# Kernel tuning notes

Hardware: AMD Instinct MI355X
Metric: run time of the kernel (lower is better)

The kernel has to match this reference:

```python
import jax, jax.numpy as jnp
import numpy as np

B, S, D_IN = 32, 4096, 256
D, T, NB, K = 256, 256, 4, 5  # d_model, compressed_len, n_blocks, kernel_size
EPS = 1e-5


def setup_inputs() -> dict:
    key = jax.random.key(0)
    ks = jax.random.split(key, 20)
    x = jax.random.normal(ks[0], (B, S, D_IN), jnp.float32)
    # ragged valid-prefix lengths in [1, S]
    lengths = jax.random.randint(ks[1], (B,), 1, S + 1)
    mask = jnp.arange(S)[None, :] < lengths[:, None]  # bool [B,S]
    sc = 0.02
    inp = {
        'x': x,
        'mask': mask,
        'in_w': jax.random.normal(ks[2], (D_IN, D), jnp.float32) * sc,
        'in_b': jnp.zeros((D,), jnp.float32),
        'ln_g': jnp.ones((NB, D), jnp.float32),
        'ln_b': jnp.zeros((NB, D), jnp.float32),
        'dw_w': jax.random.normal(ks[3], (NB, D, 1, K), jnp.float32) * sc,
        'dw_b': jnp.zeros((NB, D), jnp.float32),
        'win_w': jax.random.normal(ks[4], (NB, D, 2 * D), jnp.float32) * sc,
        'win_b': jnp.zeros((NB, 2 * D), jnp.float32),
        'wout_w': jax.random.normal(ks[5], (NB, D, D), jnp.float32) * sc,
        'wout_b': jnp.zeros((NB, D), jnp.float32),
        'fn_g': jnp.ones((D,), jnp.float32),
        'fn_b': jnp.zeros((D,), jnp.float32),
    }
    return inp


def layer_norm(h, g, b):
    mu = jnp.mean(h, axis=-1, keepdims=True)
    var = jnp.mean((h - mu) ** 2, axis=-1, keepdims=True)
    return (h - mu) * jax.lax.rsqrt(var + EPS) * g + b


def compress(x, mask, target_len):
    # Vectorized equivalent of the per-sample F.interpolate(mode='linear',
    # align_corners=False) loop: src = (j+0.5)*(L/T) - 0.5, clamped, lerp.
    lengths = mask.astype(jnp.int32).sum(axis=1)  # [B]
    Lf = lengths.astype(x.dtype)
    j = jnp.arange(target_len, dtype=x.dtype)
    src = (j[None, :] + 0.5) * (Lf[:, None] / target_len) - 0.5  # [B,T]
    src = jnp.clip(src, 0.0, jnp.maximum(Lf[:, None] - 1.0, 0.0))
    i0 = jnp.floor(src).astype(jnp.int32)
    i1 = jnp.minimum(i0 + 1, jnp.maximum(lengths[:, None] - 1, 0))
    w = (src - i0.astype(x.dtype))[..., None]  # [B,T,1]
    gather = jax.vmap(lambda xb, ib: xb[ib])  # [S,D],[T] -> [T,D]
    out = (1.0 - w) * gather(x, i0) + w * gather(x, i1)  # [B,T,D]
    valid = lengths > 0
    out = jnp.where(valid[:, None, None], out, 0.0)
    comp_mask = jnp.broadcast_to(valid[:, None], (x.shape[0], target_len))
    return out, comp_mask


def conv_block(h, g, b, dww, dwb, winw, winb, woutw, woutb):
    residual = h
    hn = layer_norm(h, g, b)
    hc = jax.lax.conv_general_dilated(
        hn.transpose(0, 2, 1), dww, window_strides=(1,),
        padding=[(K // 2, K // 2)], dimension_numbers=('NCW', 'OIW', 'NCW'),
        feature_group_count=D)
    hc = hc.transpose(0, 2, 1) + dwb  # [B,T,D]
    gv = hc @ winw + winb
    gate, val = jnp.split(gv, 2, axis=-1)
    h2 = jax.nn.sigmoid(gate) * jax.nn.gelu(val, approximate=False)
    return residual + h2 @ woutw + woutb


def reference(x, mask, in_w, in_b, ln_g, ln_b, dw_w, dw_b, win_w, win_b,
              wout_w, wout_b, fn_g, fn_b):
    xc, comp_mask = compress(x, mask, T)
    h = xc @ in_w + in_b
    for i in range(NB):
        h = conv_block(h, ln_g[i], ln_b[i], dw_w[i], dw_b[i], win_w[i],
                       win_b[i], wout_w[i], wout_b[i])
    return layer_norm(h, fn_g, fn_b), comp_mask
```

## Files before the change

kernel.cpp:

```cpp
#include <hip/hip_runtime.h>
#include <math.h>

#define B_    32
#define S_    4096
#define DIN_  256
#define D_    256
#define T_    256
#define NB_   4
#define K_    5
#define EPS_  1e-5f
#define ROWS_ (B_ * T_)

#define MROWS 32
#define GROWS 36
#define ASTR  264

typedef short  shortx8 __attribute__((ext_vector_type(8)));
typedef float  floatx4 __attribute__((ext_vector_type(4)));

__device__ __forceinline__ unsigned short f2bf(float f) {
    unsigned int u = __float_as_uint(f);
    u += 0x7FFFu + ((u >> 16) & 1u);
    return (unsigned short)(u >> 16);
}
__device__ __forceinline__ float bf2f(unsigned short h) {
    return __uint_as_float(((unsigned int)h) << 16);
}

__global__ void k_setup(const float* __restrict__ in_w, const float* __restrict__ win_w,
                        const float* __restrict__ wout_w, const unsigned int* __restrict__ mask_w,
                        unsigned short* __restrict__ wt_in, unsigned short* __restrict__ wt_win,
                        unsigned short* __restrict__ wt_wout, int* __restrict__ lengths) {
    int z = blockIdx.z;
    int tid = threadIdx.x;

    if (z == 9) {
        int b = blockIdx.y * 16 + blockIdx.x;
        if (b >= B_) return;
        int mode = 0;
        unsigned int w0 = mask_w[0];
        if (w0 == 0x3F800000u) mode = 2;
        else {
            bool u8 = false;
            for (int i = 0; i < 32; ++i)
                if (mask_w[i * 1024] > 1u) { u8 = true; break; }
            mode = u8 ? 1 : 0;
        }
        int s = 0;
        if (mode == 0) {
            const int* m = (const int*)mask_w;
            for (int i = tid; i < S_; i += 256) s += (m[(size_t)b * S_ + i] != 0);
        } else if (mode == 2) {
            const float* m = (const float*)mask_w;
            for (int i = tid; i < S_; i += 256) s += (m[(size_t)b * S_ + i] != 0.0f);
        } else {
            const unsigned char* m = (const unsigned char*)mask_w;
            for (int i = tid; i < S_; i += 256) s += (m[(size_t)b * S_ + i] != 0);
        }
        __shared__ int sm[256];
        sm[tid] = s;
        __syncthreads();
        for (int off = 128; off > 0; off >>= 1) {
            if (tid < off) sm[tid] += sm[tid + off];
            __syncthreads();
        }
        if (tid == 0) lengths[b] = sm[0];
        return;
    }

    const float* src; unsigned short* dst; int N, Kd;
    if (z == 0)      { src = in_w;                                   dst = wt_in;                                   N = D_;     Kd = DIN_; }
    else if (z <= 4) { src = win_w  + (size_t)(z - 1) * D_ * 2 * D_; dst = wt_win  + (size_t)(z - 1) * 2 * D_ * D_; N = 2 * D_; Kd = D_; }
    else             { src = wout_w + (size_t)(z - 5) * D_ * D_;     dst = wt_wout + (size_t)(z - 5) * D_ * D_;     N = D_;     Kd = D_; }
    int bx = blockIdx.x * 32;
    int by = blockIdx.y * 32;
    if (bx >= N) return;
    __shared__ float tile[32][33];
    int tx = tid & 31, ty = tid >> 5;
#pragma unroll
    for (int i = 0; i < 32; i += 8)
        tile[ty + i][tx] = src[(size_t)(by + ty + i) * N + bx + tx];
    __syncthreads();
#pragma unroll
    for (int i = 0; i < 32; i += 8)
        dst[(size_t)(bx + ty + i) * Kd + by + tx] = f2bf(tile[tx][ty + i]);
}

template<bool INIT>
__device__ __forceinline__ void gemm2(
    const unsigned short (*A)[ASTR], const unsigned short* __restrict__ wt,
    const float* __restrict__ bias, float (&hreg)[2][2][4],
    int w, int c16, int q)
{
#pragma unroll
    for (int nn = 0; nn < 2; ++nn) {
        int nt = w + nn * 8;
        const unsigned short* wp = wt + (size_t)(nt * 16 + c16) * 256 + q * 8;
        shortx8 Bf[8];
#pragma unroll
        for (int kk = 0; kk < 8; ++kk) Bf[kk] = *(const shortx8*)(wp + kk * 32);
        floatx4 acc[2] = {};
#pragma unroll
        for (int kk = 0; kk < 8; ++kk) {
#pragma unroll
            for (int mt = 0; mt < 2; ++mt) {
                shortx8 a = *(const shortx8*)&A[2 + mt * 16 + c16][kk * 32 + q * 8];
                acc[mt] = __builtin_amdgcn_mfma_f32_16x16x32_bf16(a, Bf[kk], acc[mt], 0, 0, 0);
            }
        }
        float ob = bias[nt * 16 + c16];
#pragma unroll
        for (int mt = 0; mt < 2; ++mt)
#pragma unroll
            for (int r = 0; r < 4; ++r) {
                float v = acc[mt][r] + ob;
                if (INIT) hreg[nn][mt][r] = v; else hreg[nn][mt][r] += v;
            }
    }
}

__device__ __forceinline__ void stats_pass(
    const float (&hreg)[2][2][4], float2* st,
    float (*rowS)[MROWS], float (*rowSS)[MROWS],
    int tid, int w, int c16, int q)
{
#pragma unroll
    for (int mt = 0; mt < 2; ++mt)
#pragma unroll
        for (int r = 0; r < 4; ++r) {
            float v0 = hreg[0][mt][r], v1 = hreg[1][mt][r];
            float s = v0 + v1, ss = v0 * v0 + v1 * v1;
#pragma unroll
            for (int off = 1; off < 16; off <<= 1) {
                s += __shfl_xor(s, off);
                ss += __shfl_xor(ss, off);
            }
            if (c16 == 0) {
                rowS[w][mt * 16 + q * 4 + r] = s;
                rowSS[w][mt * 16 + q * 4 + r] = ss;
            }
        }
    __syncthreads();
    if (tid < MROWS) {
        float s = 0.f, ss = 0.f;
#pragma unroll
        for (int i = 0; i < 8; ++i) { s += rowS[i][tid]; ss += rowSS[i][tid]; }
        float mu = s * (1.0f / D_);
        float var = ss * (1.0f / D_) - mu * mu;
        st[tid] = make_float2(mu, rsqrtf(var + EPS_));
    }
    __syncthreads();
}

__global__ __launch_bounds__(512, 4) void k_mega(
    const float* __restrict__ x, const int* __restrict__ lengths,
    const unsigned short* __restrict__ wt_in, const float* __restrict__ in_b,
    const float* __restrict__ ln_g, const float* __restrict__ ln_b,
    const float* __restrict__ dw_w, const float* __restrict__ dw_b,
    const unsigned short* __restrict__ wt_win, const float* __restrict__ win_b,
    const unsigned short* __restrict__ wt_wout, const float* __restrict__ wout_b,
    const float* __restrict__ fn_g, const float* __restrict__ fn_b,
    float* __restrict__ out0, float* __restrict__ out1)
{
    __shared__ unsigned short buf0[GROWS][ASTR];
    __shared__ unsigned short buf1[GROWS][ASTR];
    __shared__ float2 st[MROWS];
    __shared__ float rowS[8][MROWS];
    __shared__ float rowSS[8][MROWS];

    int tid = threadIdx.x;
    int w = tid >> 6, lane = tid & 63;
    int c16 = lane & 15, q = lane >> 4;
    int bid = blockIdx.x;
    int b = bid >> 4, seg = bid & 15;
    int t0 = seg * 16 - 8;
    if (t0 < 0) t0 = 0;
    if (t0 > T_ - MROWS) t0 = T_ - MROWS;
    int out_lo = seg * 16;

    float hreg[2][2][4];
    int L = lengths[b];

    {
        int ccol = tid & 255, r0 = tid >> 8;
        float Lf = (float)L;
        float hi = fmaxf(Lf - 1.0f, 0.0f);
        int L1 = max(L - 1, 0);
        const float* xb = x + (size_t)b * S_ * DIN_ + ccol;
#pragma unroll
        for (int e = 0; e < 16; ++e) {
            int row = r0 + e * 2;
            int t = t0 + row;
            float src = ((float)t + 0.5f) * (Lf * (1.0f / T_)) - 0.5f;
            src = fminf(fmaxf(src, 0.0f), hi);
            int i0 = (int)floorf(src);
            int i1 = min(i0 + 1, L1);
            float wf = src - (float)i0;
            float v0 = xb[(size_t)i0 * DIN_];
            float v1 = xb[(size_t)i1 * DIN_];
            buf0[2 + row][ccol] = f2bf((1.0f - wf) * v0 + wf * v1);
        }
    }
    __syncthreads();

    gemm2<true>(buf0, wt_in, in_b, hreg, w, c16, q);

    for (int li = 0; li < NB_; ++li) {
        const float* g_i = ln_g + li * D_;
        const float* b_i = ln_b + li * D_;
        const float* dww = dw_w + li * D_ * K_;
        const float* dwb = dw_b + li * D_;
        const unsigned short* ww = wt_win + (size_t)li * 2 * D_ * D_;
        const float* wb = win_b + li * 2 * D_;
        const unsigned short* ow = wt_wout + (size_t)li * D_ * D_;
        const float* ob = wout_b + li * D_;

        stats_pass(hreg, st, rowS, rowSS, tid, w, c16, q);

#pragma unroll
        for (int nn = 0; nn < 2; ++nn) {
            int col = (w + nn * 8) * 16 + c16;
            float gg = g_i[col], bb = b_i[col];
#pragma unroll
            for (int mt = 0; mt < 2; ++mt)
#pragma unroll
                for (int r = 0; r < 4; ++r) {
                    int row = mt * 16 + q * 4 + r;
                    float2 s = st[row];
                    buf0[2 + row][col] = f2bf((hreg[nn][mt][r] - s.x) * s.y * gg + bb);
                }
        }
        {
            int idx = tid;
#pragma unroll
            for (int zz = 0; zz < 2; ++zz, idx += 512) {
                int gr = idx >> 8;
                int p = (gr < 2) ? gr : gr + 32;
                buf0[p][idx & 255] = 0;
            }
        }
        __syncthreads();

        {
            int ccol = tid & 255, r0 = tid >> 8;
            float wk[K_];
#pragma unroll
            for (int k = 0; k < K_; ++k) wk[k] = dww[ccol * K_ + k];
            float cb = dwb[ccol];
#pragma unroll
            for (int e = 0; e < 16; ++e) {
                int row = r0 + e * 2;
                float acc = cb;
#pragma unroll
                for (int k = 0; k < K_; ++k)
                    acc += bf2f(buf0[row + k][ccol]) * wk[k];
                buf1[2 + row][ccol] = f2bf(acc);
            }
        }
        __syncthreads();

        float gvreg[4][2][4];
#pragma unroll
        for (int nn = 0; nn < 4; ++nn) {
            int nt = w + nn * 8;
            const unsigned short* wp = ww + (size_t)(nt * 16 + c16) * 256 + q * 8;
            shortx8 Bf[8];
#pragma unroll
            for (int kk = 0; kk < 8; ++kk) Bf[kk] = *(const shortx8*)(wp + kk * 32);
            floatx4 acc[2] = {};
#pragma unroll
            for (int kk = 0; kk < 8; ++kk) {
#pragma unroll
                for (int mt = 0; mt < 2; ++mt) {
                    shortx8 a = *(const shortx8*)&buf1[2 + mt * 16 + c16][kk * 32 + q * 8];
                    acc[mt] = __builtin_amdgcn_mfma_f32_16x16x32_bf16(a, Bf[kk], acc[mt], 0, 0, 0);
                }
            }
            float bb = wb[nt * 16 + c16];
#pragma unroll
            for (int mt = 0; mt < 2; ++mt)
#pragma unroll
                for (int r = 0; r < 4; ++r) gvreg[nn][mt][r] = acc[mt][r] + bb;
        }

#pragma unroll
        for (int pp = 0; pp < 2; ++pp) {
            int col = (w + pp * 8) * 16 + c16;
#pragma unroll
            for (int mt = 0; mt < 2; ++mt)
#pragma unroll
                for (int r = 0; r < 4; ++r) {
                    float gate = gvreg[pp][mt][r];
                    float val  = gvreg[pp + 2][mt][r];
                    float sg = 1.0f / (1.0f + __expf(-gate));
                    float u = 1.5957691216f * (val + 0.044715f * val * val * val);
                    float ge = val / (1.0f + __expf(-u));
                    buf0[2 + mt * 16 + q * 4 + r][col] = f2bf(sg * ge);
                }
        }
        __syncthreads();

        gemm2<false>(buf0, ow, ob, hreg, w, c16, q);
    }

    stats_pass(hreg, st, rowS, rowSS, tid, w, c16, q);
#pragma unroll
    for (int nn = 0; nn < 2; ++nn) {
        int col = (w + nn * 8) * 16 + c16;
        float gg = fn_g[col], bb = fn_b[col];
#pragma unroll
        for (int mt = 0; mt < 2; ++mt)
#pragma unroll
            for (int r = 0; r < 4; ++r) {
                int row = mt * 16 + q * 4 + r;
                int t = t0 + row;
                int tl = t - out_lo;
                if (tl >= 0 && tl < 16) {
                    float2 s = st[row];
                    out0[((size_t)b * T_ + t) * D_ + col] =
                        (hreg[nn][mt][r] - s.x) * s.y * gg + bb;
                }
            }
    }
    if (tid < 16) out1[(size_t)b * T_ + out_lo + tid] = 1.0f;
}

extern "C" void kernel_launch(void* const* d_in, const int* in_sizes, int n_in,
                              void* d_out, int out_size, void* d_ws, size_t ws_size,
                              hipStream_t stream) {
    const float* x      = (const float*)d_in[0];
    const unsigned int* mask_w = (const unsigned int*)d_in[1];
    const float* in_w   = (const float*)d_in[2];
    const float* in_b   = (const float*)d_in[3];
    const float* ln_g   = (const float*)d_in[4];
    const float* ln_b   = (const float*)d_in[5];
    const float* dw_w   = (const float*)d_in[6];
    const float* dw_b   = (const float*)d_in[7];
    const float* win_w  = (const float*)d_in[8];
    const float* win_b  = (const float*)d_in[9];
    const float* wout_w = (const float*)d_in[10];
    const float* wout_b = (const float*)d_in[11];
    const float* fn_g   = (const float*)d_in[12];
    const float* fn_b   = (const float*)d_in[13];

    char* w8 = (char*)d_ws;
    unsigned short* wt_in   = (unsigned short*)w8;
    unsigned short* wt_win  = wt_in  + (size_t)D_ * DIN_;
    unsigned short* wt_wout = wt_win + (size_t)NB_ * 2 * D_ * D_;
    int* lengths = (int*)(w8 + (4u << 20));

    float* out0 = (float*)d_out;
    float* out1 = out0 + (size_t)ROWS_ * D_;

    k_setup<<<dim3(16, 8, 10), 256, 0, stream>>>(in_w, win_w, wout_w, mask_w,
                                                 wt_in, wt_win, wt_wout, lengths);
    k_mega<<<512, 512, 0, stream>>>(x, lengths, wt_in, in_b, ln_g, ln_b, dw_w, dw_b,
                                    wt_win, win_b, wt_wout, wout_b, fn_g, fn_b,
                                    out0, out1);
}
```

Baseline: 312.8 us.

## Split fused mega-kernel into per-block kernels with global h and halo exchange

Replaces the single fused kernel, which used overlapping 32-row tiles (16 useful rows plus halo) so each block could carry the whole 4-block stack, with a front kernel and one kernel per conv block. Activations round-trip through global fp32 buffers, and each block recomputes LayerNorm for its 2-row halo. This removes the redundant halo compute (half the rows were wasted) and halves the grid. It also prefetches the next weight fragments while the current MFMA tile runs and packs the depthwise conv into two columns per thread. The cost is extra global traffic per layer and five launches, at lower occupancy (launch bounds 2).

```diff
diff --git a/kernel.cpp b/kernel.cpp
--- a/kernel.cpp
+++ b/kernel.cpp
@@ -11,8 +11,8 @@
 #define EPS_  1e-5f
 #define ROWS_ (B_ * T_)
 
-#define MROWS 32
-#define GROWS 36
+#define ORS_  32
+#define HR_   36
 #define ASTR  264
 
 typedef short  shortx8 __attribute__((ext_vector_type(8)));
@@ -23,8 +23,11 @@
     u += 0x7FFFu + ((u >> 16) & 1u);
     return (unsigned short)(u >> 16);
 }
-__device__ __forceinline__ float bf2f(unsigned short h) {
-    return __uint_as_float(((unsigned int)h) << 16);
+__device__ __forceinline__ float bf2f_lo(unsigned int u) {
+    return __uint_as_float(u << 16);
+}
+__device__ __forceinline__ float bf2f_hi(unsigned int u) {
+    return __uint_as_float(u & 0xFFFF0000u);
 }
 
 __global__ void k_setup(const float* __restrict__ in_w, const float* __restrict__ win_w,
@@ -86,107 +89,24 @@
         dst[(size_t)(bx + ty + i) * Kd + by + tx] = f2bf(tile[tx][ty + i]);
 }
 
-template<bool INIT>
-__device__ __forceinline__ void gemm2(
-    const unsigned short (*A)[ASTR], const unsigned short* __restrict__ wt,
-    const float* __restrict__ bias, float (&hreg)[2][2][4],
-    int w, int c16, int q)
-{
-#pragma unroll
-    for (int nn = 0; nn < 2; ++nn) {
-        int nt = w + nn * 8;
-        const unsigned short* wp = wt + (size_t)(nt * 16 + c16) * 256 + q * 8;
-        shortx8 Bf[8];
-#pragma unroll
-        for (int kk = 0; kk < 8; ++kk) Bf[kk] = *(const shortx8*)(wp + kk * 32);
-        floatx4 acc[2] = {};
-#pragma unroll
-        for (int kk = 0; kk < 8; ++kk) {
-#pragma unroll
-            for (int mt = 0; mt < 2; ++mt) {
-                shortx8 a = *(const shortx8*)&A[2 + mt * 16 + c16][kk * 32 + q * 8];
-                acc[mt] = __builtin_amdgcn_mfma_f32_16x16x32_bf16(a, Bf[kk], acc[mt], 0, 0, 0);
-            }
-        }
-        float ob = bias[nt * 16 + c16];
-#pragma unroll
-        for (int mt = 0; mt < 2; ++mt)
-#pragma unroll
-            for (int r = 0; r < 4; ++r) {
-                float v = acc[mt][r] + ob;
-                if (INIT) hreg[nn][mt][r] = v; else hreg[nn][mt][r] += v;
-            }
-    }
-}
-
-__device__ __forceinline__ void stats_pass(
-    const float (&hreg)[2][2][4], float2* st,
-    float (*rowS)[MROWS], float (*rowSS)[MROWS],
-    int tid, int w, int c16, int q)
-{
-#pragma unroll
-    for (int mt = 0; mt < 2; ++mt)
-#pragma unroll
-        for (int r = 0; r < 4; ++r) {
-            float v0 = hreg[0][mt][r], v1 = hreg[1][mt][r];
-            float s = v0 + v1, ss = v0 * v0 + v1 * v1;
-#pragma unroll
-            for (int off = 1; off < 16; off <<= 1) {
-                s += __shfl_xor(s, off);
-                ss += __shfl_xor(ss, off);
-            }
-            if (c16 == 0) {
-                rowS[w][mt * 16 + q * 4 + r] = s;
-                rowSS[w][mt * 16 + q * 4 + r] = ss;
-            }
-        }
-    __syncthreads();
-    if (tid < MROWS) {
-        float s = 0.f, ss = 0.f;
-#pragma unroll
-        for (int i = 0; i < 8; ++i) { s += rowS[i][tid]; ss += rowSS[i][tid]; }
-        float mu = s * (1.0f / D_);
-        float var = ss * (1.0f / D_) - mu * mu;
-        st[tid] = make_float2(mu, rsqrtf(var + EPS_));
-    }
-    __syncthreads();
-}
-
-__global__ __launch_bounds__(512, 4) void k_mega(
+__global__ __launch_bounds__(512, 2) void k_front(
     const float* __restrict__ x, const int* __restrict__ lengths,
     const unsigned short* __restrict__ wt_in, const float* __restrict__ in_b,
-    const float* __restrict__ ln_g, const float* __restrict__ ln_b,
-    const float* __restrict__ dw_w, const float* __restrict__ dw_b,
-    const unsigned short* __restrict__ wt_win, const float* __restrict__ win_b,
-    const unsigned short* __restrict__ wt_wout, const float* __restrict__ wout_b,
-    const float* __restrict__ fn_g, const float* __restrict__ fn_b,
-    float* __restrict__ out0, float* __restrict__ out1)
+    float* __restrict__ h0)
 {
-    __shared__ unsigned short buf0[GROWS][ASTR];
-    __shared__ unsigned short buf1[GROWS][ASTR];
-    __shared__ float2 st[MROWS];
-    __shared__ float rowS[8][MROWS];
-    __shared__ float rowSS[8][MROWS];
-
+    __shared__ unsigned short bufC[ORS_][ASTR];
     int tid = threadIdx.x;
     int w = tid >> 6, lane = tid & 63;
     int c16 = lane & 15, q = lane >> 4;
-    int bid = blockIdx.x;
-    int b = bid >> 4, seg = bid & 15;
-    int t0 = seg * 16 - 8;
-    if (t0 < 0) t0 = 0;
-    if (t0 > T_ - MROWS) t0 = T_ - MROWS;
-    int out_lo = seg * 16;
-
-    float hreg[2][2][4];
+    int b = blockIdx.x >> 3, seg = blockIdx.x & 7;
+    int t0 = seg * ORS_;
     int L = lengths[b];
-
     {
-        int ccol = tid & 255, r0 = tid >> 8;
+        int col = tid & 255, r0 = tid >> 8;
         float Lf = (float)L;
         float hi = fmaxf(Lf - 1.0f, 0.0f);
         int L1 = max(L - 1, 0);
-        const float* xb = x + (size_t)b * S_ * DIN_ + ccol;
+        const float* xb = x + (size_t)b * S_ * DIN_ + col;
 #pragma unroll
         for (int e = 0; e < 16; ++e) {
             int row = r0 + e * 2;
@@ -198,131 +118,268 @@
             float wf = src - (float)i0;
             float v0 = xb[(size_t)i0 * DIN_];
             float v1 = xb[(size_t)i1 * DIN_];
-            buf0[2 + row][ccol] = f2bf((1.0f - wf) * v0 + wf * v1);
+            bufC[row][col] = f2bf((1.0f - wf) * v0 + wf * v1);
         }
     }
     __syncthreads();
-
-    gemm2<true>(buf0, wt_in, in_b, hreg, w, c16, q);
-
-    for (int li = 0; li < NB_; ++li) {
-        const float* g_i = ln_g + li * D_;
-        const float* b_i = ln_b + li * D_;
-        const float* dww = dw_w + li * D_ * K_;
-        const float* dwb = dw_b + li * D_;
-        const unsigned short* ww = wt_win + (size_t)li * 2 * D_ * D_;
-        const float* wb = win_b + li * 2 * D_;
-        const unsigned short* ow = wt_wout + (size_t)li * D_ * D_;
-        const float* ob = wout_b + li * D_;
-
-        stats_pass(hreg, st, rowS, rowSS, tid, w, c16, q);
-
+#pragma unroll
+    for (int nn = 0; nn < 2; ++nn) {
+        int nt = w + nn * 8;
+        const unsigned short* wp = wt_in + (size_t)(nt * 16 + c16) * 256 + q * 8;
+        shortx8 Bf[8];
+#pragma unroll
+        for (int kk = 0; kk < 8; ++kk) Bf[kk] = *(const shortx8*)(wp + kk * 32);
+        floatx4 acc[2] = {};
+#pragma unroll
+        for (int kk = 0; kk < 8; ++kk)
+#pragma unroll
+            for (int mt = 0; mt < 2; ++mt) {
+                shortx8 a = *(const shortx8*)&bufC[mt * 16 + c16][kk * 32 + q * 8];
+                acc[mt] = __builtin_amdgcn_mfma_f32_16x16x32_bf16(a, Bf[kk], acc[mt], 0, 0, 0);
+            }
+        float ob = in_b[nt * 16 + c16];
+#pragma unroll
+        for (int mt = 0; mt < 2; ++mt)
+#pragma unroll
+            for (int r = 0; r < 4; ++r) {
+                int row = mt * 16 + q * 4 + r;
+                h0[((size_t)b * T_ + t0 + row) * D_ + nt * 16 + c16] = acc[mt][r] + ob;
+            }
+    }
+}
+
+__global__ __launch_bounds__(512, 2) void k_blk(
+    const float* __restrict__ hin, float* __restrict__ hout,
+    const float* __restrict__ g_i, const float* __restrict__ b_i,
+    const float* __restrict__ dww, const float* __restrict__ dwb,
+    const unsigned short* __restrict__ ww, const float* __restrict__ wb,
+    const unsigned short* __restrict__ ow, const float* __restrict__ ob,
+    const float* __restrict__ fn_g, const float* __restrict__ fn_b,
+    float* __restrict__ out0, float* __restrict__ out1, int last)
+{
+    __shared__ unsigned short buf0[HR_][ASTR];
+    __shared__ unsigned short buf1[ORS_][ASTR];
+    __shared__ float2 st[ORS_];
+    __shared__ float rowS[8][ORS_];
+    __shared__ float rowSS[8][ORS_];
+
+    int tid = threadIdx.x;
+    int w = tid >> 6, lane = tid & 63;
+    int c16 = lane & 15, q = lane >> 4;
+    int b = blockIdx.x >> 3, seg = blockIdx.x & 7;
+    int t0 = seg * ORS_;
+
+    {
+        float gv4[4], bv4[4];
+#pragma unroll
+        for (int i = 0; i < 4; ++i) { gv4[i] = g_i[lane + 64 * i]; bv4[i] = b_i[lane + 64 * i]; }
+        float vv[5][4];
+#pragma unroll
+        for (int it = 0; it < 5; ++it) {
+            int r = w + it * 8;
+            int t = t0 - 2 + r;
+            bool ok = (r < HR_) && (t >= 0) && (t < T_);
+            int tc = min(max(t, 0), T_ - 1);
+            const float* hp = hin + ((size_t)b * T_ + tc) * D_ + lane;
+#pragma unroll
+            for (int i = 0; i < 4; ++i) {
+                float v = hp[64 * i];
+                vv[it][i] = ok ? v : 0.0f;
+            }
+        }
+#pragma unroll
+        for (int it = 0; it < 5; ++it) {
+            int r = w + it * 8;
+            if (r < HR_) {
+                float s  = vv[it][0] + vv[it][1] + vv[it][2] + vv[it][3];
+                float ss = vv[it][0] * vv[it][0] + vv[it][1] * vv[it][1]
+                         + vv[it][2] * vv[it][2] + vv[it][3] * vv[it][3];
+#pragma unroll
+                for (int off = 1; off < 64; off <<= 1) {
+                    s += __shfl_xor(s, off);
+                    ss += __shfl_xor(ss, off);
+                }
+                float mu = s * (1.0f / D_);
+                float rsig = rsqrtf(ss * (1.0f / D_) - mu * mu + EPS_);
+                int t = t0 - 2 + r;
+                bool okt = (t >= 0) && (t < T_);
+#pragma unroll
+                for (int i = 0; i < 4; ++i) {
+                    float ln = (vv[it][i] - mu) * rsig * gv4[i] + bv4[i];
+                    buf0[r][lane + 64 * i] = okt ? f2bf(ln) : (unsigned short)0;
+                }
+            }
+        }
+    }
+    shortx8 Bf[8];
+    {
+        const unsigned short* wp = ww + (size_t)(w * 16 + c16) * 256 + q * 8;
+#pragma unroll
+        for (int kk = 0; kk < 8; ++kk) Bf[kk] = *(const shortx8*)(wp + kk * 32);
+    }
+    __syncthreads();
+
+    {
+        int cp = tid & 127;
+        int rg = tid >> 7;
+        int col = cp * 2;
+        float wk0[K_], wk1[K_];
+#pragma unroll
+        for (int k = 0; k < K_; ++k) { wk0[k] = dww[col * K_ + k]; wk1[k] = dww[(col + 1) * K_ + k]; }
+        float cb0 = dwb[col], cb1 = dwb[col + 1];
+#pragma unroll
+        for (int e = 0; e < 8; ++e) {
+            int rr = rg + e * 4;
+            float a0 = cb0, a1 = cb1;
+#pragma unroll
+            for (int k = 0; k < K_; ++k) {
+                unsigned int u = *(const unsigned int*)&buf0[rr + k][col];
+                a0 += bf2f_lo(u) * wk0[k];
+                a1 += bf2f_hi(u) * wk1[k];
+            }
+            unsigned int o = ((unsigned int)f2bf(a0)) | (((unsigned int)f2bf(a1)) << 16);
+            *(unsigned int*)&buf1[rr][col] = o;
+        }
+    }
+    __syncthreads();
+
+    float gvreg[4][2][4];
+#pragma unroll
+    for (int nn = 0; nn < 4; ++nn) {
+        shortx8 Bn[8];
+        if (nn < 3) {
+            const unsigned short* wp = ww + (size_t)((w + (nn + 1) * 8) * 16 + c16) * 256 + q * 8;
+#pragma unroll
+            for (int kk = 0; kk < 8; ++kk) Bn[kk] = *(const shortx8*)(wp + kk * 32);
+        } else {
+            const unsigned short* wp = ow + (size_t)(w * 16 + c16) * 256 + q * 8;
+#pragma unroll
+            for (int kk = 0; kk < 8; ++kk) Bn[kk] = *(const shortx8*)(wp + kk * 32);
+        }
+        floatx4 acc[2] = {};
+#pragma unroll
+        for (int kk = 0; kk < 8; ++kk)
+#pragma unroll
+            for (int mt = 0; mt < 2; ++mt) {
+                shortx8 a = *(const shortx8*)&buf1[mt * 16 + c16][kk * 32 + q * 8];
+                acc[mt] = __builtin_amdgcn_mfma_f32_16x16x32_bf16(a, Bf[kk], acc[mt], 0, 0, 0);
+            }
+        float bb = wb[(w + nn * 8) * 16 + c16];
+#pragma unroll
+        for (int mt = 0; mt < 2; ++mt)
+#pragma unroll
+            for (int r = 0; r < 4; ++r) gvreg[nn][mt][r] = acc[mt][r] + bb;
+#pragma unroll
+        for (int kk = 0; kk < 8; ++kk) Bf[kk] = Bn[kk];
+    }
+#pragma unroll
+    for (int pp = 0; pp < 2; ++pp) {
+        int colw = (w + pp * 8) * 16 + c16;
+#pragma unroll
+        for (int mt = 0; mt < 2; ++mt)
+#pragma unroll
+            for (int r = 0; r < 4; ++r) {
+                float gate = gvreg[pp][mt][r];
+                float val  = gvreg[pp + 2][mt][r];
+                float sg = 1.0f / (1.0f + __expf(-gate));
+                float u = 1.5957691216f * (val + 0.044715f * val * val * val);
+                float ge = val / (1.0f + __expf(-u));
+                buf0[mt * 16 + q * 4 + r][colw] = f2bf(sg * ge);
+            }
+    }
+    __syncthreads();
+
+    float vreg[2][2][4];
+#pragma unroll
+    for (int nn = 0; nn < 2; ++nn) {
+        int nt = w + nn * 8;
+        shortx8 Bn[8];
+        if (nn == 0) {
+            const unsigned short* wp = ow + (size_t)((w + 8) * 16 + c16) * 256 + q * 8;
+#pragma unroll
+            for (int kk = 0; kk < 8; ++kk) Bn[kk] = *(const shortx8*)(wp + kk * 32);
+        }
+        float res[2][4];
+#pragma unroll
+        for (int mt = 0; mt < 2; ++mt)
+#pragma unroll
+            for (int r = 0; r < 4; ++r) {
+                int row = mt * 16 + q * 4 + r;
+                res[mt][r] = hin[((size_t)b * T_ + t0 + row) * D_ + nt * 16 + c16];
+            }
+        floatx4 acc[2] = {};
+#pragma unroll
+        for (int kk = 0; kk < 8; ++kk)
+#pragma unroll
+            for (int mt = 0; mt < 2; ++mt) {
+                shortx8 a = *(const shortx8*)&buf0[mt * 16 + c16][kk * 32 + q * 8];
+                acc[mt] = __builtin_amdgcn_mfma_f32_16x16x32_bf16(a, Bf[kk], acc[mt], 0, 0, 0);
+            }
+        float bb = ob[nt * 16 + c16];
+#pragma unroll
+        for (int mt = 0; mt < 2; ++mt)
+#pragma unroll
+            for (int r = 0; r < 4; ++r)
+                vreg[nn][mt][r] = res[mt][r] + acc[mt][r] + bb;
+        if (nn == 0) {
+#pragma unroll
+            for (int kk = 0; kk < 8; ++kk) Bf[kk] = Bn[kk];
+        }
+    }
+
+    if (!last) {
+#pragma unroll
+        for (int nn = 0; nn < 2; ++nn)
+#pragma unroll
+            for (int mt = 0; mt < 2; ++mt)
+#pragma unroll
+                for (int r = 0; r < 4; ++r) {
+                    int row = mt * 16 + q * 4 + r;
+                    hout[((size_t)b * T_ + t0 + row) * D_ + (w + nn * 8) * 16 + c16] = vreg[nn][mt][r];
+                }
+    } else {
+#pragma unroll
+        for (int mt = 0; mt < 2; ++mt)
+#pragma unroll
+            for (int r = 0; r < 4; ++r) {
+                float s = vreg[0][mt][r] + vreg[1][mt][r];
+                float ss = vreg[0][mt][r] * vreg[0][mt][r] + vreg[1][mt][r] * vreg[1][mt][r];
+#pragma unroll
+                for (int off = 1; off < 16; off <<= 1) {
+                    s += __shfl_xor(s, off);
+                    ss += __shfl_xor(ss, off);
+                }
+                if (c16 == 0) {
+                    rowS[w][mt * 16 + q * 4 + r] = s;
+                    rowSS[w][mt * 16 + q * 4 + r] = ss;
+                }
+            }
+        __syncthreads();
+        if (tid < ORS_) {
+            float s = 0.f, ss = 0.f;
+#pragma unroll
+            for (int i = 0; i < 8; ++i) { s += rowS[i][tid]; ss += rowSS[i][tid]; }
+            float mu = s * (1.0f / D_);
+            float var = ss * (1.0f / D_) - mu * mu;
+            st[tid] = make_float2(mu, rsqrtf(var + EPS_));
+        }
+        __syncthreads();
 #pragma unroll
         for (int nn = 0; nn < 2; ++nn) {
             int col = (w + nn * 8) * 16 + c16;
-            float gg = g_i[col], bb = b_i[col];
+            float gg = fn_g[col], bb = fn_b[col];
 #pragma unroll
             for (int mt = 0; mt < 2; ++mt)
 #pragma unroll
                 for (int r = 0; r < 4; ++r) {
                     int row = mt * 16 + q * 4 + r;
-                    float2 s = st[row];
-                    buf0[2 + row][col] = f2bf((hreg[nn][mt][r] - s.x) * s.y * gg + bb);
-                }
-        }
-        {
-            int idx = tid;
-#pragma unroll
-            for (int zz = 0; zz < 2; ++zz, idx += 512) {
-                int gr = idx >> 8;
-                int p = (gr < 2) ? gr : gr + 32;
-                buf0[p][idx & 255] = 0;
-            }
-        }
-        __syncthreads();
-
-        {
-            int ccol = tid & 255, r0 = tid >> 8;
-            float wk[K_];
-#pragma unroll
-            for (int k = 0; k < K_; ++k) wk[k] = dww[ccol * K_ + k];
-            float cb = dwb[ccol];
-#pragma unroll
-            for (int e = 0; e < 16; ++e) {
-                int row = r0 + e * 2;
-                float acc = cb;
-#pragma unroll
-                for (int k = 0; k < K_; ++k)
-                    acc += bf2f(buf0[row + k][ccol]) * wk[k];
-                buf1[2 + row][ccol] = f2bf(acc);
-            }
-        }
-        __syncthreads();
-
-        float gvreg[4][2][4];
-#pragma unroll
-        for (int nn = 0; nn < 4; ++nn) {
-            int nt = w + nn * 8;
-            const unsigned short* wp = ww + (size_t)(nt * 16 + c16) * 256 + q * 8;
-            shortx8 Bf[8];
-#pragma unroll
-            for (int kk = 0; kk < 8; ++kk) Bf[kk] = *(const shortx8*)(wp + kk * 32);
-            floatx4 acc[2] = {};
-#pragma unroll
-            for (int kk = 0; kk < 8; ++kk) {
-#pragma unroll
-                for (int mt = 0; mt < 2; ++mt) {
-                    shortx8 a = *(const shortx8*)&buf1[2 + mt * 16 + c16][kk * 32 + q * 8];
-                    acc[mt] = __builtin_amdgcn_mfma_f32_16x16x32_bf16(a, Bf[kk], acc[mt], 0, 0, 0);
-                }
-            }
-            float bb = wb[nt * 16 + c16];
-#pragma unroll
-            for (int mt = 0; mt < 2; ++mt)
-#pragma unroll
-                for (int r = 0; r < 4; ++r) gvreg[nn][mt][r] = acc[mt][r] + bb;
-        }
-
-#pragma unroll
-        for (int pp = 0; pp < 2; ++pp) {
-            int col = (w + pp * 8) * 16 + c16;
-#pragma unroll
-            for (int mt = 0; mt < 2; ++mt)
-#pragma unroll
-                for (int r = 0; r < 4; ++r) {
-                    float gate = gvreg[pp][mt][r];
-                    float val  = gvreg[pp + 2][mt][r];
-                    float sg = 1.0f / (1.0f + __expf(-gate));
-                    float u = 1.5957691216f * (val + 0.044715f * val * val * val);
-                    float ge = val / (1.0f + __expf(-u));
-                    buf0[2 + mt * 16 + q * 4 + r][col] = f2bf(sg * ge);
-                }
-        }
-        __syncthreads();
-
-        gemm2<false>(buf0, ow, ob, hreg, w, c16, q);
-    }
-
-    stats_pass(hreg, st, rowS, rowSS, tid, w, c16, q);
-#pragma unroll
-    for (int nn = 0; nn < 2; ++nn) {
-        int col = (w + nn * 8) * 16 + c16;
-        float gg = fn_g[col], bb = fn_b[col];
-#pragma unroll
-        for (int mt = 0; mt < 2; ++mt)
-#pragma unroll
-            for (int r = 0; r < 4; ++r) {
-                int row = mt * 16 + q * 4 + r;
-                int t = t0 + row;
-                int tl = t - out_lo;
-                if (tl >= 0 && tl < 16) {
-                    float2 s = st[row];
-                    out0[((size_t)b * T_ + t) * D_ + col] =
-                        (hreg[nn][mt][r] - s.x) * s.y * gg + bb;
-                }
-            }
-    }
-    if (tid < 16) out1[(size_t)b * T_ + out_lo + tid] = 1.0f;
+                    float2 sv = st[row];
+                    out0[((size_t)b * T_ + t0 + row) * D_ + col] =
+                        (vreg[nn][mt][r] - sv.x) * sv.y * gg + bb;
+                }
+        }
+        if (tid < ORS_) out1[(size_t)b * T_ + t0 + tid] = 1.0f;
+    }
 }
 
 extern "C" void kernel_launch(void* const* d_in, const int* in_sizes, int n_in,
@@ -347,14 +404,26 @@
     unsigned short* wt_in   = (unsigned short*)w8;
     unsigned short* wt_win  = wt_in  + (size_t)D_ * DIN_;
     unsigned short* wt_wout = wt_win + (size_t)NB_ * 2 * D_ * D_;
-    int* lengths = (int*)(w8 + (4u << 20));
+    int* lengths = (int*)(w8 + (2u << 20));
+    float* h0 = (float*)(w8 + (4u << 20));
+    float* h1 = (float*)(w8 + (12u << 20));
 
     float* out0 = (float*)d_out;
     float* out1 = out0 + (size_t)ROWS_ * D_;
 
     k_setup<<<dim3(16, 8, 10), 256, 0, stream>>>(in_w, win_w, wout_w, mask_w,
                                                  wt_in, wt_win, wt_wout, lengths);
-    k_mega<<<512, 512, 0, stream>>>(x, lengths, wt_in, in_b, ln_g, ln_b, dw_w, dw_b,
-                                    wt_win, win_b, wt_wout, wout_b, fn_g, fn_b,
-                                    out0, out1);
-}
+    k_front<<<256, 512, 0, stream>>>(x, lengths, wt_in, in_b, h0);
+
+    for (int li = 0; li < NB_; ++li) {
+        const float* hin = (li & 1) ? h1 : h0;
+        float* hout      = (li & 1) ? h0 : h1;
+        k_blk<<<256, 512, 0, stream>>>(
+            hin, hout,
+            ln_g + li * D_, ln_b + li * D_,
+            dw_w + li * D_ * K_, dw_b + li * D_,
+            wt_win + (size_t)li * 2 * D_ * D_, win_b + li * 2 * D_,
+            wt_wout + (size_t)li * D_ * D_, wout_b + li * D_,
+            fn_g, fn_b, out0, out1, li == 3 ? 1 : 0);
+    }
+}
```

Result: faster. 293.3 us (-6.2%).
